# Kernel optimization log

Measured on AMD Instinct MI355X. Metric: run time of the kernel, lower is better.

The kernel has to match this reference:

```python
import jax, jax.numpy as jnp
import numpy as np

B, C, T, H, HB, E, EH, TH = 512, 30, 3, 512, 512, 6, 512, 512
SCALE = 0.02
LOSS_COEF = 0.01


def setup_inputs() -> dict:
    key = jax.random.key(0)
    ks = jax.random.split(key, 12)
    return {
        "candidate_cls_embed": jax.random.normal(ks[0], (B, C, H), jnp.float32),
        "scores": jax.random.uniform(ks[1], (B, T, C), dtype=jnp.float32),
        "fc1_w": jax.random.normal(ks[2], (H, HB), jnp.float32) * SCALE,
        "fc1_b": jnp.zeros((HB,), jnp.float32),
        "fc2_w": jax.random.normal(ks[3], (HB, H), jnp.float32) * SCALE,
        "fc2_b": jnp.zeros((H,), jnp.float32),
        "w_gate": jax.random.normal(ks[4], (T, H, E), jnp.float32) * SCALE,
        "expert_w1": jax.random.normal(ks[5], (E, H, EH), jnp.float32) * SCALE,
        "expert_b1": jnp.zeros((E, EH), jnp.float32),
        "expert_w2": jax.random.normal(ks[6], (E, EH, H), jnp.float32) * SCALE,
        "expert_b2": jnp.zeros((E, H), jnp.float32),
        "tower_w1": jax.random.normal(ks[7], (T, H, TH), jnp.float32) * SCALE,
        "tower_b1": jnp.zeros((T, TH), jnp.float32),
        "tower_w2": jax.random.normal(ks[8], (T, TH), jnp.float32) * SCALE,
        "tower_b2": jnp.zeros((T,), jnp.float32),
        "k": 3,
    }


def reference(candidate_cls_embed, scores, fc1_w, fc1_b, fc2_w, fc2_b, w_gate,
              expert_w1, expert_b1, expert_w2, expert_b2,
              tower_w1, tower_b1, tower_w2, tower_b2, k):
    n_experts = w_gate.shape[-1]
    n_tasks = scores.shape[1]

    # labels: 1 where score hits the per-task max (non-differentiable construction)
    labels = jax.lax.stop_gradient(
        (scores == scores.max(axis=-1, keepdims=True)).astype(scores.dtype))  # [B,T,C]

    # shared bottom: fc2(relu(fc1(x)))
    h = jax.nn.relu(candidate_cls_embed @ fc1_w + fc1_b) @ fc2_w + fc2_b  # [B,C,H]

    # per-task top-k gating (MMoE style)
    glog = jnp.einsum('bch,the->btce', h, w_gate)                 # [B,T,C,E]
    topv, topi = jax.lax.top_k(glog, k)                           # [B,T,C,k]
    topg = jax.nn.softmax(topv, axis=-1)                          # softmax over kept experts
    gates = jnp.sum(topg[..., None] * jax.nn.one_hot(topi, n_experts, dtype=topg.dtype),
                    axis=-2)                                      # [B,T,C,E]

    # all-expert MLPs (dense over E; E is small)
    eh = jax.nn.relu(jnp.einsum('bch,ehf->bcef', h, expert_w1) + expert_b1)  # [B,C,E,EH]
    eo = jnp.einsum('bcef,efh->bceh', eh, expert_w2) + expert_b2             # [B,C,E,H]

    # gated combination per task
    y = jnp.einsum('btce,bceh->btch', gates, eo)                  # [B,T,C,H]

    # per-task towers -> one logit per candidate
    th = jax.nn.relu(jnp.einsum('btch,thf->btcf', y, tower_w1) + tower_b1[None, :, None, :])
    logits = jnp.einsum('btcf,tf->btc', th, tower_w2) + tower_b2[None, :, None]  # [B,T,C]

    # BCE-with-logits, mean over candidates, mean over tasks
    bce = jnp.maximum(logits, 0.0) - logits * labels + jnp.log1p(jnp.exp(-jnp.abs(logits)))
    task_loss = bce.mean(axis=-1).mean(axis=-1)                   # [B]

    # aux load-balancing loss: cv^2 of per-expert importance per sample/task
    imp = gates.sum(axis=2)                                       # [B,T,E]
    cv2 = imp.var(axis=-1) / (imp.mean(axis=-1) ** 2 + 1e-10)     # [B,T]
    aux = LOSS_COEF * cv2.sum(axis=-1)                            # [B]

    loss = (task_loss + aux).mean()
    return loss
```

## Files before the change

### kernel.cpp

```cpp
#include <hip/hip_runtime.h>
#include <hip/hip_bf16.h>
#include <cstdint>
#include <cstddef>

typedef unsigned short u16;
typedef unsigned char u8;
typedef long i64;
typedef __bf16 bf16x8 __attribute__((ext_vector_type(8)));
typedef float f32x4 __attribute__((ext_vector_type(4)));
typedef u16 u16x8 __attribute__((ext_vector_type(8)));
typedef u8 u8x16 __attribute__((ext_vector_type(16)));
typedef i64 i64x2 __attribute__((ext_vector_type(2)));

#define NROWS 15360
#define KDIM 512
#define BDIM 512
#define CDIM 30
#define TDIM 3
#define EDIM 6

typedef __attribute__((address_space(1))) const unsigned int gu32;
typedef __attribute__((address_space(3))) unsigned int lu32;

__device__ __forceinline__ void gload16(const void* g, void* l) {
  __builtin_amdgcn_global_load_lds((gu32*)g, (lu32*)l, 16, 0, 0);
}

__device__ __forceinline__ float bf2f(u16 u) {
  union { unsigned i; float f; } v; v.i = ((unsigned)u) << 16; return v.f;
}
__device__ __forceinline__ u16 f2bf(float f) {
  union { float f; unsigned i; } v; v.f = f;
  unsigned r = v.i + 0x7fffu + ((v.i >> 16) & 1u);
  return (u16)(r >> 16);
}
__device__ __forceinline__ u8 f2fp8_sw(float v) {
  union { float f; unsigned u; } x; x.f = v;
  unsigned s = (x.u >> 24) & 0x80;
  x.u &= 0x7fffffffu;
  if (x.f < 0.0009765625f) return (u8)s;
  if (x.f > 448.f) return (u8)(s | 0x7e);
  int e; float m = frexpf(x.f, &e);
  if (e < -5) {
    int qq = (int)(x.f * 512.f + 0.5f);
    return (u8)(s | qq);
  }
  int qq = (int)(m * 16.f + 0.5f);
  if (qq == 16) { qq = 8; e++; }
  int E = e + 6;
  if (E >= 16 || (E == 15 && qq - 8 == 7)) return (u8)(s | 0x7e);
  return (u8)(s | (E << 3) | (qq - 8));
}
__device__ __forceinline__ unsigned cvt2fp8(float a, float b) {
#if __has_builtin(__builtin_amdgcn_cvt_pk_fp8_f32)
  return (unsigned)__builtin_amdgcn_cvt_pk_fp8_f32(a, b, 0, false) & 0xffffu;
#else
  return (unsigned)f2fp8_sw(a) | ((unsigned)f2fp8_sw(b) << 8);
#endif
}
__device__ __forceinline__ int permpos(int j) {
  return ((j & 24) << 1) + ((j & 32) >> 2) + (j & 7);
}

__global__ __launch_bounds__(256) void prep_kernel(
    const float* __restrict__ X, u16* __restrict__ Xb,
    const float* __restrict__ fc1, const float* __restrict__ fc2,
    const float* __restrict__ ew1, const float* __restrict__ ew2,
    const float* __restrict__ tw1, u16* __restrict__ wt,
    u8* __restrict__ w1q, u8* __restrict__ w2q, u8* __restrict__ tw1q,
    const float* __restrict__ wg, u16* __restrict__ WgT,
    float* __restrict__ logits) {
  int bid = blockIdx.x;
  if (bid < 3840) {
    int i = (bid * 256 + threadIdx.x) * 8;
    float4 a = *(const float4*)(X + i);
    float4 b = *(const float4*)(X + i + 4);
    u16x8 v;
    v[0] = f2bf(a.x); v[1] = f2bf(a.y); v[2] = f2bf(a.z); v[3] = f2bf(a.w);
    v[4] = f2bf(b.x); v[5] = f2bf(b.y); v[6] = f2bf(b.z); v[7] = f2bf(b.w);
    *(u16x8*)(Xb + i) = v;
  } else if (bid < 4928) {
    int id = bid - 3840;
    int mid = id >> 6, tile = id & 63;
    const float* src;
    if (mid == 0) src = fc1;
    else if (mid == 1) src = fc2;
    else if (mid < 8) src = ew1 + (size_t)(mid - 2) * 262144;
    else if (mid < 14) src = ew2 + (size_t)(mid - 8) * 262144;
    else src = tw1 + (size_t)(mid - 14) * 262144;
    int tr = (tile >> 3) * 64, tc = (tile & 7) * 64;
    __shared__ float t[64][65];
    int c = threadIdx.x & 63, r0 = threadIdx.x >> 6;
#pragma unroll
    for (int i = 0; i < 16; i++) {
      int r = r0 + i * 4;
      t[r][c] = src[(size_t)(tr + r) * 512 + tc + c];
    }
    __syncthreads();
    if (mid >= 2) {
      u8* dq;
      if (mid < 8) dq = w1q + (size_t)(mid - 2) * 262144;
      else if (mid < 14) dq = w2q + (size_t)(mid - 8) * 262144;
      else dq = tw1q + (size_t)(mid - 14) * 262144;
      int pc = tr + permpos(c);
#pragma unroll
      for (int i = 0; i < 16; i++) {
        int r = r0 + i * 4;
        dq[(size_t)(tc + r) * 512 + pc] = (u8)(cvt2fp8(t[c][r] * 64.f, 0.f) & 0xff);
      }
    } else {
      u16* dst = wt + (size_t)mid * 262144;
#pragma unroll
      for (int i = 0; i < 16; i++) {
        int r = r0 + i * 4;
        dst[(size_t)(tc + r) * 512 + tr + c] = f2bf(t[c][r]);
      }
    }
  } else if (bid < 4960) {
    int col = bid - 4928;
    for (int k = threadIdx.x; k < 512; k += 256) {
      u16 v = 0;
      if (col < 18) {
        int t = col / 6, e = col % 6;
        v = f2bf(wg[(size_t)(t * 512 + k) * 6 + e]);
      }
      WgT[(size_t)col * 512 + k] = v;
    }
  } else {
    int i = (bid - 4960) * 1024 + threadIdx.x * 4;
    float4 z; z.x = 0.f; z.y = 0.f; z.z = 0.f; z.w = 0.f;
    *(float4*)(logits + i) = z;
  }
}

__global__ __launch_bounds__(256) void cvt_h_kernel(const u16* __restrict__ h,
                                                    u8* __restrict__ hq) {
  int idx = blockIdx.x * 256 + threadIdx.x;
  int row = idx >> 3, g = idx & 7;
  const u16* src = h + (size_t)row * 512 + g * 64;
  u8 outb[64];
#pragma unroll
  for (int c = 0; c < 8; c++) {
    u16x8 v = *(const u16x8*)(src + c * 8);
    int base = (c & 3) * 16 + (c & 4) * 2;
#pragma unroll
    for (int t = 0; t < 8; t += 2) {
      unsigned p = cvt2fp8(bf2f(v[t]) * 16.f, bf2f(v[t + 1]) * 16.f);
      outb[base + t] = (u8)(p & 0xff);
      outb[base + t + 1] = (u8)(p >> 8);
    }
  }
  u8* dst = hq + (size_t)row * 512 + g * 64;
#pragma unroll
  for (int j = 0; j < 4; j++)
    *(u8x16*)(dst + j * 16) = *(const u8x16*)&outb[j * 16];
}

__global__ __launch_bounds__(512, 4) void gemm256q(
    const u8* __restrict__ Aq,
    const u8* __restrict__ Bq,
    const float* __restrict__ bias,
    u8* __restrict__ Cq,
    int nby) {
  int nwg = gridDim.x;
  int cpx = nwg >> 3;
  int bid = blockIdx.x;
  int swz = (bid & 7) * cpx + (bid >> 3);
  int bx = swz / nby, by = swz % nby;
  int brow = bx * 128, bcol = by * 256;

  __shared__ __align__(16) u8 SB8[3][24576];

  int tid = threadIdx.x, lane = tid & 63, w = tid >> 6;
  int wm = w >> 2, wn = w & 3;
  int l = lane & 15, q = lane >> 4;

  int srow = tid >> 2, sc = tid & 3;
  int scX = sc ^ ((srow >> 1) & 3);
  const u8* Ag = Aq + (size_t)(brow + srow) * 512 + scX * 16;
  const u8* Bg0 = Bq + (size_t)(bcol + srow) * 512 + scX * 16;
  const u8* Bg1 = Bg0 + (size_t)128 * 512;
  int lo = w * 1024;

#define STAGEQ(buf, kt)                                \
  do {                                                 \
    gload16(Ag + (kt) * 64, (buf) + lo);               \
    gload16(Bg0 + (kt) * 64, (buf) + 8192 + lo);       \
    gload16(Bg1 + (kt) * 64, (buf) + 16384 + lo);      \
  } while (0)

  f32x4 acc[4][4];
#pragma unroll
  for (int m = 0; m < 4; m++)
#pragma unroll
    for (int n = 0; n < 4; n++) {
      acc[m][n][0] = 0.f; acc[m][n][1] = 0.f; acc[m][n][2] = 0.f; acc[m][n][3] = 0.f;
    }

  int xg = q ^ ((l >> 1) & 3);

  STAGEQ(SB8[0], 0);
  STAGEQ(SB8[1], 1);
  asm volatile("s_waitcnt vmcnt(3)" ::: "memory");
  __builtin_amdgcn_s_barrier();

  u8 *bc = SB8[0], *bn = SB8[1], *bq = SB8[2];
#pragma unroll
  for (int kt = 0; kt < 8; ++kt) {
    if (kt < 6) STAGEQ(bq, kt + 2);
    i64x2 afv[4], bfv[4];
#pragma unroll
    for (int mi = 0; mi < 4; mi++) {
      int row = wm * 64 + mi * 16 + l;
      afv[mi] = *(const i64x2*)&bc[row * 64 + xg * 16];
    }
#pragma unroll
    for (int ni = 0; ni < 4; ni++) {
      int col = wn * 64 + ni * 16 + l;
      bfv[ni] = *(const i64x2*)&bc[8192 + col * 64 + xg * 16];
    }
    __builtin_amdgcn_s_setprio(1);
#pragma unroll
    for (int ks = 0; ks < 2; ++ks)
#pragma unroll
      for (int mi = 0; mi < 4; mi++)
#pragma unroll
        for (int ni = 0; ni < 4; ni++)
          acc[mi][ni] = __builtin_amdgcn_mfma_f32_16x16x32_fp8_fp8(
              afv[mi][ks], bfv[ni][ks], acc[mi][ni], 0, 0, 0);
    __builtin_amdgcn_s_setprio(0);
    asm volatile("s_waitcnt lgkmcnt(0)" ::: "memory");
    if (kt < 6)
      asm volatile("s_waitcnt vmcnt(3)" ::: "memory");
    else
      asm volatile("s_waitcnt vmcnt(0)" ::: "memory");
    __builtin_amdgcn_s_barrier();
    u8* t_ = bc; bc = bn; bn = bq; bq = t_;
  }
#undef STAGEQ

  u8* S8 = (u8*)&SB8[0][0];
  float bvs[4];
#pragma unroll
  for (int n = 0; n < 4; n++) bvs[n] = bias[bcol + wn * 64 + n * 16 + l];
#pragma unroll
  for (int m = 0; m < 4; m++) {
    int rl = wm * 64 + m * 16 + q * 4;
#pragma unroll
    for (int n = 0; n < 4; n++) {
      int pc = wn * 64 + permpos(n * 16 + l);
      float v0 = fmaxf(acc[m][n][0] * 9.765625e-4f + bvs[n], 0.f) * 16.f;
      float v1 = fmaxf(acc[m][n][1] * 9.765625e-4f + bvs[n], 0.f) * 16.f;
      float v2 = fmaxf(acc[m][n][2] * 9.765625e-4f + bvs[n], 0.f) * 16.f;
      float v3 = fmaxf(acc[m][n][3] * 9.765625e-4f + bvs[n], 0.f) * 16.f;
      unsigned p01 = cvt2fp8(v0, v1);
      unsigned p23 = cvt2fp8(v2, v3);
      S8[(rl + 0) * 264 + pc] = (u8)(p01 & 0xff);
      S8[(rl + 1) * 264 + pc] = (u8)(p01 >> 8);
      S8[(rl + 2) * 264 + pc] = (u8)(p23 & 0xff);
      S8[(rl + 3) * 264 + pc] = (u8)(p23 >> 8);
    }
  }
  __syncthreads();
  int row = tid >> 2, cc = tid & 3;
#pragma unroll
  for (int j = 0; j < 4; j++)
    *(u8x16*)&Cq[(size_t)(brow + row) * 3072 + bcol + cc * 64 + j * 16] =
        *(const u8x16*)&S8[row * 264 + cc * 64 + j * 16];
}

__global__ __launch_bounds__(256, 2) void gemm_w2c(
    const u8* __restrict__ eh,
    const u8* __restrict__ W2q,
    const float* __restrict__ eb2,
    const float* __restrict__ gates,
    u8* __restrict__ yq) {
  int nwg = gridDim.x, cpx = nwg >> 3;
  int bid = blockIdx.x;
  int swz = (bid & 7) * cpx + (bid >> 3);
  int bx = swz >> 2, by = swz & 3;
  int brow = bx * 64, bcol = by * 128;

  __shared__ __align__(16) u8 SB8[3][12288];
  __shared__ u16 glds[64 * 18];

  int tid = threadIdx.x, lane = tid & 63, w = tid >> 6;
  int l = lane & 15, q = lane >> 4;

  for (int i = tid; i < 64 * 18; i += 256) {
    int r = i / 18, te = i % 18;
    int gr = brow + r, b = gr / CDIM, c = gr % CDIM;
    int t = te / 6, e = te % 6;
    glds[i] = f2bf(gates[((size_t)(b * TDIM + t) * CDIM + c) * EDIM + e]);
  }
  float b2all[2][6];
#pragma unroll
  for (int ni = 0; ni < 2; ni++) {
    int col = bcol + w * 32 + ni * 16 + l;
#pragma unroll
    for (int e = 0; e < 6; e++) b2all[ni][e] = eb2[e * 512 + col];
  }

  int srow = tid >> 2, sc = tid & 3;
  int scX = sc ^ ((srow >> 1) & 3);
  const u8* Ag = eh + (size_t)(brow + srow) * 3072 + scX * 16;
  const u8* Bg0 = W2q + (size_t)(bcol + srow) * 512 + scX * 16;
  const u8* Bg1 = Bg0 + (size_t)64 * 512;
  int lo = w * 1024;

#define STAGEW(buf, s2)                                                   \
  do {                                                                    \
    int _e2 = (s2) >> 3, _k2 = (s2) & 7;                                  \
    gload16(Ag + _e2 * 512 + _k2 * 64, (buf) + lo);                       \
    gload16(Bg0 + (size_t)_e2 * 262144 + _k2 * 64, (buf) + 4096 + lo);    \
    gload16(Bg1 + (size_t)_e2 * 262144 + _k2 * 64, (buf) + 8192 + lo);    \
  } while (0)

  f32x4 P[4][2], aY0[4][2], aY1[4][2], aY2[4][2];
#pragma unroll
  for (int mi = 0; mi < 4; mi++)
#pragma unroll
    for (int ni = 0; ni < 2; ni++) {
      P[mi][ni][0] = P[mi][ni][1] = P[mi][ni][2] = P[mi][ni][3] = 0.f;
      aY0[mi][ni] = P[mi][ni]; aY1[mi][ni] = P[mi][ni]; aY2[mi][ni] = P[mi][ni];
    }

  int xg = q ^ ((l >> 1) & 3);

  STAGEW(SB8[0], 0);
  STAGEW(SB8[1], 1);
  asm volatile("s_waitcnt vmcnt(3)" ::: "memory");
  __builtin_amdgcn_s_barrier();

  u8 *bc = SB8[0], *bn = SB8[1], *bq = SB8[2];
  for (int e = 0; e < 6; ++e) {
#pragma unroll
    for (int kt = 0; kt < 8; ++kt) {
      int s = e * 8 + kt;
      if (s < 46) STAGEW(bq, s + 2);
      i64x2 bfv[2], afv[4];
#pragma unroll
      for (int ni = 0; ni < 2; ni++) {
        int col = w * 32 + ni * 16 + l;
        bfv[ni] = *(const i64x2*)&bc[4096 + col * 64 + xg * 16];
      }
#pragma unroll
      for (int mi = 0; mi < 4; mi++) {
        int row = mi * 16 + l;
        afv[mi] = *(const i64x2*)&bc[row * 64 + xg * 16];
      }
      __builtin_amdgcn_s_setprio(1);
#pragma unroll
      for (int ks = 0; ks < 2; ++ks)
#pragma unroll
        for (int mi = 0; mi < 4; mi++)
#pragma unroll
          for (int ni = 0; ni < 2; ni++)
            P[mi][ni] = __builtin_amdgcn_mfma_f32_16x16x32_fp8_fp8(
                afv[mi][ks], bfv[ni][ks], P[mi][ni], 0, 0, 0);
      __builtin_amdgcn_s_setprio(0);
      asm volatile("s_waitcnt lgkmcnt(0)" ::: "memory");
      if (s < 46)
        asm volatile("s_waitcnt vmcnt(3)" ::: "memory");
      else
        asm volatile("s_waitcnt vmcnt(0)" ::: "memory");
      __builtin_amdgcn_s_barrier();
      u8* t_ = bc; bc = bn; bn = bq; bq = t_;
    }
#pragma unroll
    for (int mi = 0; mi < 4; mi++) {
#pragma unroll
      for (int rr = 0; rr < 4; rr++) {
        int row = mi * 16 + q * 4 + rr;
        float g0 = bf2f(glds[row * 18 + e]);
        float g1 = bf2f(glds[row * 18 + 6 + e]);
        float g2 = bf2f(glds[row * 18 + 12 + e]);
#pragma unroll
        for (int ni = 0; ni < 2; ni++) {
          float p = P[mi][ni][rr] * 9.765625e-4f + b2all[ni][e];
          aY0[mi][ni][rr] += g0 * p;
          aY1[mi][ni][rr] += g1 * p;
          aY2[mi][ni][rr] += g2 * p;
          P[mi][ni][rr] = 0.f;
        }
      }
    }
  }
#undef STAGEW

  u8* S8 = (u8*)&SB8[0][0];
#define EPI(AY, t)                                                          \
  do {                                                                      \
    _Pragma("unroll") for (int mi = 0; mi < 4; mi++) {                      \
      int rl = mi * 16 + q * 4;                                             \
      _Pragma("unroll") for (int ni = 0; ni < 2; ni++) {                    \
        int colL = w * 32 + ni * 16 + l;                                    \
        int pc = (colL & 64) + permpos(colL & 63);                          \
        unsigned p01 = cvt2fp8(AY[mi][ni][0] * 32.f, AY[mi][ni][1] * 32.f); \
        unsigned p23 = cvt2fp8(AY[mi][ni][2] * 32.f, AY[mi][ni][3] * 32.f); \
        S8[(rl + 0) * 144 + pc] = (u8)(p01 & 0xff);                         \
        S8[(rl + 1) * 144 + pc] = (u8)(p01 >> 8);                           \
        S8[(rl + 2) * 144 + pc] = (u8)(p23 & 0xff);                         \
        S8[(rl + 3) * 144 + pc] = (u8)(p23 >> 8);                           \
      }                                                                     \
    }                                                                       \
    __syncthreads();                                                        \
    {                                                                       \
      int row_ = tid >> 2, cc_ = tid & 3;                                   \
      _Pragma("unroll") for (int j = 0; j < 2; j++)                         \
        *(u8x16*)&yq[((size_t)(t) * NROWS + brow + row_) * 512 + bcol +     \
                     j * 64 + cc_ * 16] =                                   \
            *(const u8x16*)&S8[row_ * 144 + j * 64 + cc_ * 16];             \
    }                                                                       \
    __syncthreads();                                                        \
  } while (0)
  EPI(aY0, 0);
  EPI(aY1, 1);
  EPI(aY2, 2);
#undef EPI
}

__global__ __launch_bounds__(256, 2) void gemm_tower(
    const u8* __restrict__ yq,
    const u8* __restrict__ tw1q,
    const float* __restrict__ tb1, const float* __restrict__ tw2,
    float* __restrict__ logits) {
  int t = blockIdx.z;
  const u8* A = yq + (size_t)t * NROWS * 512;
  const u8* BT = tw1q + (size_t)t * 262144;

  int nwg = gridDim.x, cpx = nwg >> 3;
  int bid = blockIdx.x;
  int swz = (bid & 7) * cpx + (bid >> 3);
  int bx = swz >> 2, by = swz & 3;
  int brow = bx * 64, bcol = by * 128;

  __shared__ __align__(16) u8 SB8[3][12288];

  int tid = threadIdx.x, lane = tid & 63, w = tid >> 6;
  int l = lane & 15, q = lane >> 4;

  int srow = tid >> 2, sc = tid & 3;
  int scX = sc ^ ((srow >> 1) & 3);
  const u8* Ag = A + (size_t)(brow + srow) * 512 + scX * 16;
  const u8* Bg0 = BT + (size_t)(bcol + srow) * 512 + scX * 16;
  const u8* Bg1 = Bg0 + (size_t)64 * 512;
  int lo = w * 1024;

#define STAGET(buf, kt)                                \
  do {                                                 \
    gload16(Ag + (kt) * 64, (buf) + lo);               \
    gload16(Bg0 + (kt) * 64, (buf) + 4096 + lo);       \
    gload16(Bg1 + (kt) * 64, (buf) + 8192 + lo);       \
  } while (0)

  f32x4 P[4][2];
#pragma unroll
  for (int mi = 0; mi < 4; mi++)
#pragma unroll
    for (int ni = 0; ni < 2; ni++) {
      P[mi][ni][0] = 0.f; P[mi][ni][1] = 0.f; P[mi][ni][2] = 0.f; P[mi][ni][3] = 0.f;
    }

  int xg = q ^ ((l >> 1) & 3);

  STAGET(SB8[0], 0);
  STAGET(SB8[1], 1);
  asm volatile("s_waitcnt vmcnt(3)" ::: "memory");
  __builtin_amdgcn_s_barrier();

  u8 *bc = SB8[0], *bn = SB8[1], *bq = SB8[2];
#pragma unroll
  for (int kt = 0; kt < 8; ++kt) {
    if (kt < 6) STAGET(bq, kt + 2);
    i64x2 bfv[2], afv[4];
#pragma unroll
    for (int ni = 0; ni < 2; ni++) {
      int col = w * 32 + ni * 16 + l;
      bfv[ni] = *(const i64x2*)&bc[4096 + col * 64 + xg * 16];
    }
#pragma unroll
    for (int mi = 0; mi < 4; mi++) {
      int row = mi * 16 + l;
      afv[mi] = *(const i64x2*)&bc[row * 64 + xg * 16];
    }
    __builtin_amdgcn_s_setprio(1);
#pragma unroll
    for (int ks = 0; ks < 2; ++ks)
#pragma unroll
      for (int mi = 0; mi < 4; mi++)
#pragma unroll
        for (int ni = 0; ni < 2; ni++)
          P[mi][ni] = __builtin_amdgcn_mfma_f32_16x16x32_fp8_fp8(
              afv[mi][ks], bfv[ni][ks], P[mi][ni], 0, 0, 0);
    __builtin_amdgcn_s_setprio(0);
    asm volatile("s_waitcnt lgkmcnt(0)" ::: "memory");
    if (kt < 6)
      asm volatile("s_waitcnt vmcnt(3)" ::: "memory");
    else
      asm volatile("s_waitcnt vmcnt(0)" ::: "memory");
    __builtin_amdgcn_s_barrier();
    u8* t_ = bc; bc = bn; bn = bq; bq = t_;
  }
#undef STAGET

  float bvs[2], tws[2];
#pragma unroll
  for (int ni = 0; ni < 2; ni++) {
    int col = bcol + w * 32 + ni * 16 + l;
    bvs[ni] = tb1[t * 512 + col];
    tws[ni] = tw2[t * 512 + col];
  }
#pragma unroll
  for (int mi = 0; mi < 4; mi++) {
#pragma unroll
    for (int rr = 0; rr < 4; rr++) {
      float s = 0.f;
#pragma unroll
      for (int ni = 0; ni < 2; ni++) {
        float v = P[mi][ni][rr] * 4.8828125e-4f + bvs[ni];
        v = fmaxf(v, 0.f);
        s += v * tws[ni];
      }
      s += __shfl_xor(s, 1, 64);
      s += __shfl_xor(s, 2, 64);
      s += __shfl_xor(s, 4, 64);
      s += __shfl_xor(s, 8, 64);
      if (l == 0) {
        int row = brow + mi * 16 + q * 4 + rr;
        int b = row / CDIM, c = row % CDIM;
        atomicAdd(&logits[(size_t)(b * TDIM + t) * CDIM + c], s);
      }
    }
  }
}

template <int RELU>
__global__ __launch_bounds__(256, 2) void gemm_bt(
    const u16* __restrict__ A, int lda,
    const u16* __restrict__ BT,
    const float* __restrict__ bias,
    u16* __restrict__ C, int ldc) {
  __shared__ u16 S[8448];
  u16* Al = S;
  u16* Bl = S + 4096;
  int tid = threadIdx.x, lane = tid & 63, w = tid >> 6;
  int wr = w >> 1, wc = w & 1;
  int brow = blockIdx.x * 128, bcol = blockIdx.y * 128;

  int srow = tid >> 2;
  int schunk = tid & 3;
  int srcc = schunk ^ ((srow >> 1) & 3);
  const u16* Ag0 = A + (size_t)(brow + srow) * lda + srcc * 8;
  const u16* Ag1 = A + (size_t)(brow + srow + 64) * lda + srcc * 8;
  const u16* Bg0 = BT + (size_t)(bcol + srow) * KDIM + srcc * 8;
  const u16* Bg1 = BT + (size_t)(bcol + srow + 64) * KDIM + srcc * 8;
  u16* Ald0 = Al + w * 512;
  u16* Ald1 = Al + 2048 + w * 512;
  u16* Bld0 = Bl + w * 512;
  u16* Bld1 = Bl + 2048 + w * 512;

  f32x4 zero; zero[0] = 0.f; zero[1] = 0.f; zero[2] = 0.f; zero[3] = 0.f;
  f32x4 acc[4][4];
#pragma unroll
  for (int m = 0; m < 4; m++)
#pragma unroll
    for (int n = 0; n < 4; n++) acc[m][n] = zero;

  int l = lane & 15, q = lane >> 4;
  int rc = q ^ ((l >> 1) & 3);
  int rbase = wr * 64 + l;
  int cbase = wc * 64 + l;

  for (int kt = 0; kt < 16; ++kt) {
    int ko = kt * 32;
    gload16(Ag0 + ko, Ald0);
    gload16(Ag1 + ko, Ald1);
    gload16(Bg0 + ko, Bld0);
    gload16(Bg1 + ko, Bld1);
    __syncthreads();
    bf16x8 af[4], bfr[4];
#pragma unroll
    for (int m = 0; m < 4; m++) af[m] = *(const bf16x8*)&Al[(rbase + m * 16) * 32 + rc * 8];
#pragma unroll
    for (int n = 0; n < 4; n++) bfr[n] = *(const bf16x8*)&Bl[(cbase + n * 16) * 32 + rc * 8];
#pragma unroll
    for (int m = 0; m < 4; m++)
#pragma unroll
      for (int n = 0; n < 4; n++)
        acc[m][n] = __builtin_amdgcn_mfma_f32_16x16x32_bf16(af[m], bfr[n], acc[m][n], 0, 0, 0);
    __syncthreads();
  }

  int colL = wc * 64 + l;
  float bvs[4];
#pragma unroll
  for (int n = 0; n < 4; n++) bvs[n] = bias[bcol + colL + n * 16];
#pragma unroll
  for (int half = 0; half < 2; half++) {
    if (wr == half) {
#pragma unroll
      for (int m = 0; m < 4; m++) {
        int rl = m * 16 + q * 4;
#pragma unroll
        for (int n = 0; n < 4; n++) {
#pragma unroll
          for (int rr = 0; rr < 4; rr++) {
            float v = acc[m][n][rr] + bvs[n];
            if (RELU) v = fmaxf(v, 0.f);
            S[(rl + rr) * 132 + colL + n * 16] = f2bf(v);
          }
        }
      }
    }
    __syncthreads();
    int row = tid >> 2, cc = tid & 3;
#pragma unroll
    for (int j = 0; j < 4; j++)
      *(u16x8*)&C[(size_t)(brow + half * 64 + row) * ldc + bcol + cc * 32 + j * 8] =
          *(const u16x8*)&S[row * 132 + cc * 32 + j * 8];
    __syncthreads();
  }
}

__global__ __launch_bounds__(256) void gate_kernel(const u16* __restrict__ h,
                                                   const u16* __restrict__ WgT,
                                                   float* __restrict__ gates) {
  __shared__ u16 Wl[16 * 32 * 32];
  __shared__ float Gl[4][16][33];
  int tid = threadIdx.x, lane = tid & 63, w = tid >> 6;
  int l = lane & 15, q = lane >> 4;

  for (int idx = tid; idx < 2048; idx += 256) {
    int kt = idx >> 7, col = (idx >> 2) & 31, c = idx & 3;
    int sc = c ^ ((col >> 1) & 3);
    *(u16x8*)&Wl[kt * 1024 + col * 32 + c * 8] =
        *(const u16x8*)&WgT[(size_t)col * 512 + kt * 32 + sc * 8];
  }
  __syncthreads();

  int r = blockIdx.x * 64 + w * 16 + l;
  int ch = q ^ ((l >> 1) & 3);

  f32x4 acc0, acc1;
  acc0[0] = acc0[1] = acc0[2] = acc0[3] = 0.f;
  acc1 = acc0;
#pragma unroll
  for (int kt = 0; kt < 16; ++kt) {
    bf16x8 av = *(const bf16x8*)&h[(size_t)r * 512 + kt * 32 + q * 8];
    bf16x8 b0 = *(const bf16x8*)&Wl[kt * 1024 + l * 32 + ch * 8];
    bf16x8 b1 = *(const bf16x8*)&Wl[kt * 1024 + (16 + l) * 32 + ch * 8];
    acc0 = __builtin_amdgcn_mfma_f32_16x16x32_bf16(av, b0, acc0, 0, 0, 0);
    acc1 = __builtin_amdgcn_mfma_f32_16x16x32_bf16(av, b1, acc1, 0, 0, 0);
  }

#pragma unroll
  for (int rr = 0; rr < 4; rr++) {
    Gl[w][q * 4 + rr][l] = acc0[rr];
    Gl[w][q * 4 + rr][16 + l] = acc1[rr];
  }
  __syncthreads();

  if (lane < 16) {
    int R = blockIdx.x * 64 + w * 16 + lane;
    int b = R / CDIM, c = R % CDIM;
    for (int t = 0; t < 3; t++) {
      float g[6];
#pragma unroll
      for (int e = 0; e < 6; e++) g[e] = Gl[w][lane][t * 6 + e];
      float out[6] = {0, 0, 0, 0, 0, 0};
      int idx[3]; float val[3];
      unsigned used = 0;
      for (int kk = 0; kk < 3; kk++) {
        int best = 0; float bv = -1e30f;
        for (int e = 0; e < 6; e++)
          if (!((used >> e) & 1) && g[e] > bv) { bv = g[e]; best = e; }
        used |= 1u << best; idx[kk] = best; val[kk] = bv;
      }
      float mx = val[0];
      float s = 0.f, ex[3];
      for (int kk = 0; kk < 3; kk++) { ex[kk] = expf(val[kk] - mx); s += ex[kk]; }
      for (int kk = 0; kk < 3; kk++) out[idx[kk]] = ex[kk] / s;
      float* gp = &gates[(size_t)((b * TDIM + t) * CDIM + c) * EDIM];
      for (int e = 0; e < 6; e++) gp[e] = out[e];
    }
  }
}

__global__ __launch_bounds__(64) void loss_kernel(const float* __restrict__ scores,
                                                  const float* __restrict__ logits,
                                                  const float* __restrict__ gates,
                                                  const float* __restrict__ tb2,
                                                  float* __restrict__ out) {
  int b = blockIdx.x;
  int lane = threadIdx.x;
  float bce_sum = 0.f;
  float aux = 0.f;
  for (int t = 0; t < 3; t++) {
    float sc = (lane < CDIM) ? scores[(size_t)(b * TDIM + t) * CDIM + lane] : -1e30f;
    float mx = sc;
    for (int off = 32; off; off >>= 1) mx = fmaxf(mx, __shfl_xor(mx, off, 64));
    float lab = (lane < CDIM && sc == mx) ? 1.f : 0.f;
    float lg = (lane < CDIM) ? (logits[(size_t)(b * TDIM + t) * CDIM + lane] + tb2[t]) : 0.f;
    float bce = (lane < CDIM) ? (fmaxf(lg, 0.f) - lg * lab + log1pf(expf(-fabsf(lg)))) : 0.f;
    for (int off = 32; off; off >>= 1) bce += __shfl_xor(bce, off, 64);
    bce_sum += bce / (float)CDIM;

    float impv[6];
    float meansum = 0.f;
#pragma unroll
    for (int e = 0; e < 6; e++) {
      float gsum = (lane < CDIM) ? gates[(size_t)((b * TDIM + t) * CDIM + lane) * EDIM + e] : 0.f;
      for (int off = 32; off; off >>= 1) gsum += __shfl_xor(gsum, off, 64);
      impv[e] = gsum;
      meansum += gsum;
    }
    float mean = meansum / 6.f;
    float var = 0.f;
#pragma unroll
    for (int e = 0; e < 6; e++) { float d = impv[e] - mean; var += d * d; }
    var /= 6.f;
    aux += var / (mean * mean + 1e-10f);
  }
  float res = bce_sum / 3.f + 0.01f * aux;
  if (lane == 0) atomicAdd(out, res / (float)BDIM);
}

extern "C" void kernel_launch(void* const* d_in, const int* in_sizes, int n_in,
                              void* d_out, int out_size, void* d_ws, size_t ws_size,
                              hipStream_t stream) {
  const float* X = (const float*)d_in[0];
  const float* scores = (const float*)d_in[1];
  const float* fc1_w = (const float*)d_in[2];
  const float* fc1_b = (const float*)d_in[3];
  const float* fc2_w = (const float*)d_in[4];
  const float* fc2_b = (const float*)d_in[5];
  const float* w_gate = (const float*)d_in[6];
  const float* ew1 = (const float*)d_in[7];
  const float* eb1 = (const float*)d_in[8];
  const float* ew2 = (const float*)d_in[9];
  const float* eb2 = (const float*)d_in[10];
  const float* tw1 = (const float*)d_in[11];
  const float* tb1 = (const float*)d_in[12];
  const float* tw2 = (const float*)d_in[13];
  const float* tb2 = (const float*)d_in[14];
  float* out = (float*)d_out;

  u16* WT = (u16*)d_ws;
  u8* w1q = (u8*)(WT + (size_t)2 * 262144);
  u8* w2q = w1q + (size_t)6 * 262144;
  u8* tw1q = w2q + (size_t)6 * 262144;
  u16* WgT = (u16*)(tw1q + (size_t)3 * 262144);
  u8* hq = (u8*)(WgT + (size_t)32 * 512);
  u8* ehq = hq + (size_t)NROWS * 512;
  u16* Xb = (u16*)(ehq + (size_t)NROWS * 3072);
  u16* A1 = Xb + (size_t)NROWS * 512;
  u16* h = A1 + (size_t)NROWS * 512;
  u8* yq = (u8*)(h + (size_t)NROWS * 512);
  float* gates = (float*)(yq + (size_t)TDIM * NROWS * 512);
  float* logits = gates + (size_t)BDIM * TDIM * CDIM * EDIM;

  hipMemsetAsync(d_out, 0, sizeof(float) * out_size, stream);

  prep_kernel<<<5005, 256, 0, stream>>>(X, Xb, fc1_w, fc2_w, ew1, ew2, tw1, WT,
                                        w1q, w2q, tw1q, w_gate, WgT, logits);

  gemm_bt<1><<<dim3(120, 4), 256, 0, stream>>>(Xb, 512, WT + (size_t)0 * 262144, fc1_b, A1, 512);
  gemm_bt<0><<<dim3(120, 4), 256, 0, stream>>>(A1, 512, WT + (size_t)1 * 262144, fc2_b, h, 512);

  cvt_h_kernel<<<480, 256, 0, stream>>>(h, hq);

  gate_kernel<<<240, 256, 0, stream>>>(h, WgT, gates);

  gemm256q<<<dim3(1440, 1, 1), 512, 0, stream>>>(hq, w1q, eb1, ehq, 12);

  gemm_w2c<<<dim3(960, 1, 1), 256, 0, stream>>>(ehq, w2q, eb2, gates, yq);

  gemm_tower<<<dim3(960, 1, 3), 256, 0, stream>>>(yq, tw1q, tb1, tw2, logits);

  loss_kernel<<<BDIM, 64, 0, stream>>>(scores, logits, gates, tb2, out);
}
```

Measured before the change: 233.6 us.

## Quantize shared-bottom fc1/fc2 GEMMs to FP8 and fuse h quantization

Replaces the two bf16 shared-bottom GEMMs with an FP8 MFMA kernel that reads FP8-quantized input and weights produced in prep. The second GEMM writes both the FP8 hq used by the experts and the bf16 h used by the gate, which removes the separate h conversion kernel. This halves operand bytes and uses faster FP8 MFMA, at the cost of extra quantization error in fc1/fc2. That error could shift the top-k gate choices or the loss.

```diff
diff --git a/kernel.cpp b/kernel.cpp
--- a/kernel.cpp
+++ b/kernel.cpp
@@ -63,22 +63,28 @@
 }
 
 __global__ __launch_bounds__(256) void prep_kernel(
-    const float* __restrict__ X, u16* __restrict__ Xb,
+    const float* __restrict__ X, u8* __restrict__ Xq,
     const float* __restrict__ fc1, const float* __restrict__ fc2,
     const float* __restrict__ ew1, const float* __restrict__ ew2,
-    const float* __restrict__ tw1, u16* __restrict__ wt,
+    const float* __restrict__ tw1,
+    u8* __restrict__ fc1q, u8* __restrict__ fc2q,
     u8* __restrict__ w1q, u8* __restrict__ w2q, u8* __restrict__ tw1q,
     const float* __restrict__ wg, u16* __restrict__ WgT,
     float* __restrict__ logits) {
   int bid = blockIdx.x;
   if (bid < 3840) {
-    int i = (bid * 256 + threadIdx.x) * 8;
-    float4 a = *(const float4*)(X + i);
-    float4 b = *(const float4*)(X + i + 4);
-    u16x8 v;
-    v[0] = f2bf(a.x); v[1] = f2bf(a.y); v[2] = f2bf(a.z); v[3] = f2bf(a.w);
-    v[4] = f2bf(b.x); v[5] = f2bf(b.y); v[6] = f2bf(b.z); v[7] = f2bf(b.w);
-    *(u16x8*)(Xb + i) = v;
+    int i = bid * 256 + threadIdx.x;
+    float4 a = *(const float4*)(X + (size_t)i * 8);
+    float4 b = *(const float4*)(X + (size_t)i * 8 + 4);
+    unsigned p0 = cvt2fp8(a.x * 16.f, a.y * 16.f);
+    unsigned p1 = cvt2fp8(a.z * 16.f, a.w * 16.f);
+    unsigned p2 = cvt2fp8(b.x * 16.f, b.y * 16.f);
+    unsigned p3 = cvt2fp8(b.z * 16.f, b.w * 16.f);
+    int row = i >> 6, g = i & 63;
+    int pos = (g >> 3) * 64 + (g & 3) * 16 + (g & 4) * 2;
+    u8* dst = Xq + (size_t)row * 512 + pos;
+    *(unsigned*)dst = p0 | (p1 << 16);
+    *(unsigned*)(dst + 4) = p2 | (p3 << 16);
   } else if (bid < 4928) {
     int id = bid - 3840;
     int mid = id >> 6, tile = id & 63;
@@ -97,24 +103,17 @@
       t[r][c] = src[(size_t)(tr + r) * 512 + tc + c];
     }
     __syncthreads();
-    if (mid >= 2) {
-      u8* dq;
-      if (mid < 8) dq = w1q + (size_t)(mid - 2) * 262144;
-      else if (mid < 14) dq = w2q + (size_t)(mid - 8) * 262144;
-      else dq = tw1q + (size_t)(mid - 14) * 262144;
-      int pc = tr + permpos(c);
-#pragma unroll
-      for (int i = 0; i < 16; i++) {
-        int r = r0 + i * 4;
-        dq[(size_t)(tc + r) * 512 + pc] = (u8)(cvt2fp8(t[c][r] * 64.f, 0.f) & 0xff);
-      }
-    } else {
-      u16* dst = wt + (size_t)mid * 262144;
-#pragma unroll
-      for (int i = 0; i < 16; i++) {
-        int r = r0 + i * 4;
-        dst[(size_t)(tc + r) * 512 + tr + c] = f2bf(t[c][r]);
-      }
+    u8* dq;
+    if (mid == 0) dq = fc1q;
+    else if (mid == 1) dq = fc2q;
+    else if (mid < 8) dq = w1q + (size_t)(mid - 2) * 262144;
+    else if (mid < 14) dq = w2q + (size_t)(mid - 8) * 262144;
+    else dq = tw1q + (size_t)(mid - 14) * 262144;
+    int pc = tr + permpos(c);
+#pragma unroll
+    for (int i = 0; i < 16; i++) {
+      int r = r0 + i * 4;
+      dq[(size_t)(tc + r) * 512 + pc] = (u8)(cvt2fp8(t[c][r] * 64.f, 0.f) & 0xff);
     }
   } else if (bid < 4960) {
     int col = bid - 4928;
@@ -133,27 +132,146 @@
   }
 }
 
-__global__ __launch_bounds__(256) void cvt_h_kernel(const u16* __restrict__ h,
-                                                    u8* __restrict__ hq) {
-  int idx = blockIdx.x * 256 + threadIdx.x;
-  int row = idx >> 3, g = idx & 7;
-  const u16* src = h + (size_t)row * 512 + g * 64;
-  u8 outb[64];
-#pragma unroll
-  for (int c = 0; c < 8; c++) {
-    u16x8 v = *(const u16x8*)(src + c * 8);
-    int base = (c & 3) * 16 + (c & 4) * 2;
-#pragma unroll
-    for (int t = 0; t < 8; t += 2) {
-      unsigned p = cvt2fp8(bf2f(v[t]) * 16.f, bf2f(v[t + 1]) * 16.f);
-      outb[base + t] = (u8)(p & 0xff);
-      outb[base + t + 1] = (u8)(p >> 8);
-    }
-  }
-  u8* dst = hq + (size_t)row * 512 + g * 64;
-#pragma unroll
-  for (int j = 0; j < 4; j++)
-    *(u8x16*)(dst + j * 16) = *(const u8x16*)&outb[j * 16];
+template <int DUAL>
+__global__ __launch_bounds__(256, 2) void gemm_s8(
+    const u8* __restrict__ Aq,
+    const u8* __restrict__ Bq,
+    const float* __restrict__ bias,
+    u8* __restrict__ Cq,
+    u16* __restrict__ Ch) {
+  int nwg = gridDim.x, cpx = nwg >> 3;
+  int bid = blockIdx.x;
+  int swz = (bid & 7) * cpx + (bid >> 3);
+  int bx = swz >> 2, by = swz & 3;
+  int brow = bx * 64, bcol = by * 128;
+
+  __shared__ __align__(16) u8 SB8[3][12288];
+
+  int tid = threadIdx.x, lane = tid & 63, w = tid >> 6;
+  int l = lane & 15, q = lane >> 4;
+
+  int srow = tid >> 2, sc = tid & 3;
+  int scX = sc ^ ((srow >> 1) & 3);
+  const u8* Ag = Aq + (size_t)(brow + srow) * 512 + scX * 16;
+  const u8* Bg0 = Bq + (size_t)(bcol + srow) * 512 + scX * 16;
+  const u8* Bg1 = Bg0 + (size_t)64 * 512;
+  int lo = w * 1024;
+
+#define STAGES(buf, kt)                                \
+  do {                                                 \
+    gload16(Ag + (kt) * 64, (buf) + lo);               \
+    gload16(Bg0 + (kt) * 64, (buf) + 4096 + lo);       \
+    gload16(Bg1 + (kt) * 64, (buf) + 8192 + lo);       \
+  } while (0)
+
+  f32x4 P[4][2];
+#pragma unroll
+  for (int mi = 0; mi < 4; mi++)
+#pragma unroll
+    for (int ni = 0; ni < 2; ni++) {
+      P[mi][ni][0] = 0.f; P[mi][ni][1] = 0.f; P[mi][ni][2] = 0.f; P[mi][ni][3] = 0.f;
+    }
+
+  int xg = q ^ ((l >> 1) & 3);
+
+  STAGES(SB8[0], 0);
+  STAGES(SB8[1], 1);
+  asm volatile("s_waitcnt vmcnt(3)" ::: "memory");
+  __builtin_amdgcn_s_barrier();
+
+  u8 *bc = SB8[0], *bn = SB8[1], *bq = SB8[2];
+#pragma unroll
+  for (int kt = 0; kt < 8; ++kt) {
+    if (kt < 6) STAGES(bq, kt + 2);
+    i64x2 bfv[2], afv[4];
+#pragma unroll
+    for (int ni = 0; ni < 2; ni++) {
+      int col = w * 32 + ni * 16 + l;
+      bfv[ni] = *(const i64x2*)&bc[4096 + col * 64 + xg * 16];
+    }
+#pragma unroll
+    for (int mi = 0; mi < 4; mi++) {
+      int row = mi * 16 + l;
+      afv[mi] = *(const i64x2*)&bc[row * 64 + xg * 16];
+    }
+    __builtin_amdgcn_s_setprio(1);
+#pragma unroll
+    for (int ks = 0; ks < 2; ++ks)
+#pragma unroll
+      for (int mi = 0; mi < 4; mi++)
+#pragma unroll
+        for (int ni = 0; ni < 2; ni++)
+          P[mi][ni] = __builtin_amdgcn_mfma_f32_16x16x32_fp8_fp8(
+              afv[mi][ks], bfv[ni][ks], P[mi][ni], 0, 0, 0);
+    __builtin_amdgcn_s_setprio(0);
+    asm volatile("s_waitcnt lgkmcnt(0)" ::: "memory");
+    if (kt < 6)
+      asm volatile("s_waitcnt vmcnt(3)" ::: "memory");
+    else
+      asm volatile("s_waitcnt vmcnt(0)" ::: "memory");
+    __builtin_amdgcn_s_barrier();
+    u8* t_ = bc; bc = bn; bn = bq; bq = t_;
+  }
+#undef STAGES
+
+  float bvs[2];
+#pragma unroll
+  for (int ni = 0; ni < 2; ni++) bvs[ni] = bias[bcol + w * 32 + ni * 16 + l];
+
+  u8* S8 = (u8*)&SB8[0][0];
+#pragma unroll
+  for (int mi = 0; mi < 4; mi++) {
+    int rl = mi * 16 + q * 4;
+#pragma unroll
+    for (int ni = 0; ni < 2; ni++) {
+      int colL = w * 32 + ni * 16 + l;
+      int pc = (colL & 64) + permpos(colL & 63);
+      float v[4];
+#pragma unroll
+      for (int rr = 0; rr < 4; rr++) {
+        float x = P[mi][ni][rr] * 9.765625e-4f + bvs[ni];
+        if (!DUAL) x = fmaxf(x, 0.f);
+        v[rr] = x;
+      }
+      unsigned p01 = cvt2fp8(v[0] * 16.f, v[1] * 16.f);
+      unsigned p23 = cvt2fp8(v[2] * 16.f, v[3] * 16.f);
+      S8[(rl + 0) * 144 + pc] = (u8)(p01 & 0xff);
+      S8[(rl + 1) * 144 + pc] = (u8)(p01 >> 8);
+      S8[(rl + 2) * 144 + pc] = (u8)(p23 & 0xff);
+      S8[(rl + 3) * 144 + pc] = (u8)(p23 >> 8);
+    }
+  }
+  __syncthreads();
+  {
+    int row_ = tid >> 2, cc_ = tid & 3;
+#pragma unroll
+    for (int j = 0; j < 2; j++)
+      *(u8x16*)&Cq[(size_t)(brow + row_) * 512 + bcol + j * 64 + cc_ * 16] =
+          *(const u8x16*)&S8[row_ * 144 + j * 64 + cc_ * 16];
+  }
+  if (DUAL) {
+    __syncthreads();
+    u16* Sst = (u16*)&SB8[0][0];
+#pragma unroll
+    for (int mi = 0; mi < 4; mi++) {
+      int rl = mi * 16 + q * 4;
+#pragma unroll
+      for (int ni = 0; ni < 2; ni++) {
+        int colL = w * 32 + ni * 16 + l;
+#pragma unroll
+        for (int rr = 0; rr < 4; rr++) {
+          float x = P[mi][ni][rr] * 9.765625e-4f + bvs[ni];
+          Sst[(rl + rr) * 136 + colL] = f2bf(x);
+        }
+      }
+    }
+    __syncthreads();
+    int row_ = tid >> 2, cc_ = tid & 3;
+#pragma unroll
+    for (int j = 0; j < 4; j++)
+      *(u16x8*)&Ch[(size_t)(brow + row_) * 512 + bcol + cc_ * 32 + j * 8] =
+          *(const u16x8*)&Sst[row_ * 136 + cc_ * 32 + j * 8];
+  }
 }
 
 __global__ __launch_bounds__(512, 4) void gemm256q(
@@ -535,94 +653,6 @@
   }
 }
 
-template <int RELU>
-__global__ __launch_bounds__(256, 2) void gemm_bt(
-    const u16* __restrict__ A, int lda,
-    const u16* __restrict__ BT,
-    const float* __restrict__ bias,
-    u16* __restrict__ C, int ldc) {
-  __shared__ u16 S[8448];
-  u16* Al = S;
-  u16* Bl = S + 4096;
-  int tid = threadIdx.x, lane = tid & 63, w = tid >> 6;
-  int wr = w >> 1, wc = w & 1;
-  int brow = blockIdx.x * 128, bcol = blockIdx.y * 128;
-
-  int srow = tid >> 2;
-  int schunk = tid & 3;
-  int srcc = schunk ^ ((srow >> 1) & 3);
-  const u16* Ag0 = A + (size_t)(brow + srow) * lda + srcc * 8;
-  const u16* Ag1 = A + (size_t)(brow + srow + 64) * lda + srcc * 8;
-  const u16* Bg0 = BT + (size_t)(bcol + srow) * KDIM + srcc * 8;
-  const u16* Bg1 = BT + (size_t)(bcol + srow + 64) * KDIM + srcc * 8;
-  u16* Ald0 = Al + w * 512;
-  u16* Ald1 = Al + 2048 + w * 512;
-  u16* Bld0 = Bl + w * 512;
-  u16* Bld1 = Bl + 2048 + w * 512;
-
-  f32x4 zero; zero[0] = 0.f; zero[1] = 0.f; zero[2] = 0.f; zero[3] = 0.f;
-  f32x4 acc[4][4];
-#pragma unroll
-  for (int m = 0; m < 4; m++)
-#pragma unroll
-    for (int n = 0; n < 4; n++) acc[m][n] = zero;
-
-  int l = lane & 15, q = lane >> 4;
-  int rc = q ^ ((l >> 1) & 3);
-  int rbase = wr * 64 + l;
-  int cbase = wc * 64 + l;
-
-  for (int kt = 0; kt < 16; ++kt) {
-    int ko = kt * 32;
-    gload16(Ag0 + ko, Ald0);
-    gload16(Ag1 + ko, Ald1);
-    gload16(Bg0 + ko, Bld0);
-    gload16(Bg1 + ko, Bld1);
-    __syncthreads();
-    bf16x8 af[4], bfr[4];
-#pragma unroll
-    for (int m = 0; m < 4; m++) af[m] = *(const bf16x8*)&Al[(rbase + m * 16) * 32 + rc * 8];
-#pragma unroll
-    for (int n = 0; n < 4; n++) bfr[n] = *(const bf16x8*)&Bl[(cbase + n * 16) * 32 + rc * 8];
-#pragma unroll
-    for (int m = 0; m < 4; m++)
-#pragma unroll
-      for (int n = 0; n < 4; n++)
-        acc[m][n] = __builtin_amdgcn_mfma_f32_16x16x32_bf16(af[m], bfr[n], acc[m][n], 0, 0, 0);
-    __syncthreads();
-  }
-
-  int colL = wc * 64 + l;
-  float bvs[4];
-#pragma unroll
-  for (int n = 0; n < 4; n++) bvs[n] = bias[bcol + colL + n * 16];
-#pragma unroll
-  for (int half = 0; half < 2; half++) {
-    if (wr == half) {
-#pragma unroll
-      for (int m = 0; m < 4; m++) {
-        int rl = m * 16 + q * 4;
-#pragma unroll
-        for (int n = 0; n < 4; n++) {
-#pragma unroll
-          for (int rr = 0; rr < 4; rr++) {
-            float v = acc[m][n][rr] + bvs[n];
-            if (RELU) v = fmaxf(v, 0.f);
-            S[(rl + rr) * 132 + colL + n * 16] = f2bf(v);
-          }
-        }
-      }
-    }
-    __syncthreads();
-    int row = tid >> 2, cc = tid & 3;
-#pragma unroll
-    for (int j = 0; j < 4; j++)
-      *(u16x8*)&C[(size_t)(brow + half * 64 + row) * ldc + bcol + cc * 32 + j * 8] =
-          *(const u16x8*)&S[row * 132 + cc * 32 + j * 8];
-    __syncthreads();
-  }
-}
-
 __global__ __launch_bounds__(256) void gate_kernel(const u16* __restrict__ h,
                                                    const u16* __restrict__ WgT,
                                                    float* __restrict__ gates) {
@@ -746,35 +776,34 @@
   const float* tb2 = (const float*)d_in[14];
   float* out = (float*)d_out;
 
-  u16* WT = (u16*)d_ws;
-  u8* w1q = (u8*)(WT + (size_t)2 * 262144);
+  u8* fc1q = (u8*)d_ws;
+  u8* fc2q = fc1q + 262144;
+  u8* w1q = fc2q + 262144;
   u8* w2q = w1q + (size_t)6 * 262144;
   u8* tw1q = w2q + (size_t)6 * 262144;
   u16* WgT = (u16*)(tw1q + (size_t)3 * 262144);
-  u8* hq = (u8*)(WgT + (size_t)32 * 512);
-  u8* ehq = hq + (size_t)NROWS * 512;
-  u16* Xb = (u16*)(ehq + (size_t)NROWS * 3072);
-  u16* A1 = Xb + (size_t)NROWS * 512;
-  u16* h = A1 + (size_t)NROWS * 512;
-  u8* yq = (u8*)(h + (size_t)NROWS * 512);
+  u8* Xq = (u8*)(WgT + (size_t)32 * 512);
+  u8* A1q = Xq + (size_t)NROWS * 512;
+  u8* hq = A1q + (size_t)NROWS * 512;
+  u16* h = (u16*)(hq + (size_t)NROWS * 512);
+  u8* ehq = (u8*)(h + (size_t)NROWS * 512);
+  u8* yq = ehq + (size_t)NROWS * 3072;
   float* gates = (float*)(yq + (size_t)TDIM * NROWS * 512);
   float* logits = gates + (size_t)BDIM * TDIM * CDIM * EDIM;
 
   hipMemsetAsync(d_out, 0, sizeof(float) * out_size, stream);
 
-  prep_kernel<<<5005, 256, 0, stream>>>(X, Xb, fc1_w, fc2_w, ew1, ew2, tw1, WT,
-                                        w1q, w2q, tw1q, w_gate, WgT, logits);
-
-  gemm_bt<1><<<dim3(120, 4), 256, 0, stream>>>(Xb, 512, WT + (size_t)0 * 262144, fc1_b, A1, 512);
-  gemm_bt<0><<<dim3(120, 4), 256, 0, stream>>>(A1, 512, WT + (size_t)1 * 262144, fc2_b, h, 512);
-
-  cvt_h_kernel<<<480, 256, 0, stream>>>(h, hq);
+  prep_kernel<<<5005, 256, 0, stream>>>(X, Xq, fc1_w, fc2_w, ew1, ew2, tw1,
+                                        fc1q, fc2q, w1q, w2q, tw1q, w_gate, WgT, logits);
+
+  gemm_s8<0><<<dim3(960), 256, 0, stream>>>(Xq, fc1q, fc1_b, A1q, nullptr);
+  gemm_s8<1><<<dim3(960), 256, 0, stream>>>(A1q, fc2q, fc2_b, hq, h);
 
   gate_kernel<<<240, 256, 0, stream>>>(h, WgT, gates);
 
-  gemm256q<<<dim3(1440, 1, 1), 512, 0, stream>>>(hq, w1q, eb1, ehq, 12);
-
-  gemm_w2c<<<dim3(960, 1, 1), 256, 0, stream>>>(ehq, w2q, eb2, gates, yq);
+  gemm256q<<<dim3(1440), 512, 0, stream>>>(hq, w1q, eb1, ehq, 12);
+
+  gemm_w2c<<<dim3(960), 256, 0, stream>>>(ehq, w2q, eb2, gates, yq);
 
   gemm_tower<<<dim3(960, 1, 3), 256, 0, stream>>>(yq, tw1q, tb1, tw2, logits);
 
```

New measurement: 206.2 us. 1.13x faster.
